# Performance work log

Hardware: AMD Instinct MI355X
Metric: run time of the kernel (lower is better)

## Reference

```python
import jax, jax.numpy as jnp
import numpy as np

B, N, D, H, E = 8, 2048, 128, 256, 524288
EPS = 1e-5

def setup_inputs() -> dict:
    key = jax.random.key(0)
    ks = jax.random.split(key, 16)
    def lin(k, fan_in, shape):
        b = 1.0 / np.sqrt(fan_in)
        return jax.random.uniform(k, shape, jnp.float32, -b, b)
    return {
        'x': jax.random.normal(ks[0], (B, N, 3), jnp.float32),
        'h': jax.random.normal(ks[1], (B, N, D), jnp.float32),
        'edge_indices': jax.random.randint(ks[2], (2, E), 0, B * N, jnp.int64),
        'batch_size': B,
        # filter_net: Linear(1,H) -> SiLU -> Linear(H,D)   (weights stored [in,out])
        'W1': lin(ks[3], 1, (1, H)), 'b1': lin(ks[4], 1, (H,)),
        'W2': lin(ks[5], H, (H, D)), 'b2': lin(ks[6], H, (D,)),
        # update_net: Linear(2D,H) -> LayerNorm(H) -> SiLU -> Linear(H,D)
        'W3': lin(ks[7], 2 * D, (2 * D, H)), 'b3': lin(ks[8], 2 * D, (H,)),
        'gamma': jnp.ones((H,), jnp.float32), 'beta': jnp.zeros((H,), jnp.float32),
        'W4': lin(ks[9], H, (H, D)), 'b4': lin(ks[10], H, (D,)),
    }

def reference(x, h, edge_indices, batch_size, W1, b1, W2, b2, W3, b3, gamma, beta, W4, b4):
    Bn, Nn, Dn = h.shape
    row, col = edge_indices[0], edge_indices[1]
    br, nr = row // Nn, row % Nn
    bc, nc = col // Nn, col % Nn
    x_row = x[br, nr]            # [E,3] gather
    x_col = x[bc, nc]            # [E,3]
    h_col = h[bc, nc]            # [E,D]
    diff = x_row - x_col
    dist = jnp.sqrt(jnp.sum(diff * diff, axis=-1, keepdims=True))  # [E,1]
    # distance-conditioned edge filter MLP
    edge_filters = jax.nn.silu(dist @ W1 + b1) @ W2 + b2           # [E,D]
    messages = h_col * edge_filters                                 # [E,D]
    # scatter-mean into B*N nodes (single-pass sum + count, clamp_min(1))
    n_tot = Bn * Nn
    sums = jax.ops.segment_sum(messages, row, num_segments=n_tot)
    counts = jax.ops.segment_sum(jnp.ones_like(row, dtype=messages.dtype), row, num_segments=n_tot)
    agg = (sums / jnp.maximum(counts, 1.0)[:, None]).reshape(Bn, Nn, Dn)
    # update MLP with LayerNorm
    u = jnp.concatenate([h, agg], axis=-1) @ W3 + b3               # [B,N,H]
    mu = jnp.mean(u, axis=-1, keepdims=True)
    var = jnp.mean((u - mu) ** 2, axis=-1, keepdims=True)
    un = (u - mu) * jax.lax.rsqrt(var + EPS) * gamma + beta
    return jax.nn.silu(un) @ W4 + b4                                # [B,N,D]
```

## Files before the change

kernel.cpp:

```cpp
#include <hip/hip_runtime.h>
#include <hip/hip_fp16.h>
#include <math.h>

#define BN_NODES 16384
#define DIM 128
#define HID 256
#define TK 4096
#define TRANGE 32.0f
#define TSTEP (TRANGE / (float)TK)
#define TINV  ((float)TK / TRANGE)
#define LN_EPS 1e-5f
#define EPB 4096
#define NBINS 1024
#define CAPB 768

typedef _Float16 f16x8 __attribute__((ext_vector_type(8)));
typedef __attribute__((ext_vector_type(4))) float f32x4;
typedef __attribute__((ext_vector_type(2))) float floatx2;
typedef __attribute__((ext_vector_type(8))) unsigned short ushort8v;

__device__ __forceinline__ unsigned short f2h(float f) {
    _Float16 h = (_Float16)f;
    return *(unsigned short*)&h;
}
__device__ __forceinline__ unsigned char f2fp8(float f) {
    unsigned int p = __builtin_amdgcn_cvt_pk_fp8_f32(f, f, 0, false);
    return (unsigned char)(p & 0xFFu);
}

__device__ __forceinline__ void acc8(uint2 q, uint2 tv, float* a) {
    floatx2 h01 = __builtin_amdgcn_cvt_pk_f32_fp8((int)q.x, false);
    floatx2 h23 = __builtin_amdgcn_cvt_pk_f32_fp8((int)q.x, true);
    floatx2 h45 = __builtin_amdgcn_cvt_pk_f32_fp8((int)q.y, false);
    floatx2 h67 = __builtin_amdgcn_cvt_pk_f32_fp8((int)q.y, true);
    floatx2 t01 = __builtin_amdgcn_cvt_pk_f32_fp8((int)tv.x, false);
    floatx2 t23 = __builtin_amdgcn_cvt_pk_f32_fp8((int)tv.x, true);
    floatx2 t45 = __builtin_amdgcn_cvt_pk_f32_fp8((int)tv.y, false);
    floatx2 t67 = __builtin_amdgcn_cvt_pk_f32_fp8((int)tv.y, true);
    a[0] = fmaf(h01[0], t01[0], a[0]);
    a[1] = fmaf(h01[1], t01[1], a[1]);
    a[2] = fmaf(h23[0], t23[0], a[2]);
    a[3] = fmaf(h23[1], t23[1], a[3]);
    a[4] = fmaf(h45[0], t45[0], a[4]);
    a[5] = fmaf(h45[1], t45[1], a[5]);
    a[6] = fmaf(h67[0], t67[0], a[6]);
    a[7] = fmaf(h67[1], t67[1], a[7]);
}

__device__ __forceinline__ void edge_one(const unsigned int* lrec, int idx, int dd,
        const unsigned char* __restrict__ xq,
        const unsigned char* __restrict__ Tb, float* a) {
    unsigned int r0 = lrec[idx];
    int c0 = (int)((r0 >> 12) & 0x3FFFu), k0 = (int)(r0 & 0xFFFu);
    uint2 q0 = *(const uint2*)&xq[c0 * DIM + dd];
    uint2 t0 = *(const uint2*)&Tb[k0 * DIM + dd];
    acc8(q0, t0, a);
}

__global__ __launch_bounds__(256) void prep_kernel(
        const float* __restrict__ W1, const float* __restrict__ b1,
        const float* __restrict__ W2, const float* __restrict__ b2,
        const float* __restrict__ W3, const float* __restrict__ W4,
        const float* __restrict__ h, const int* __restrict__ ei,
        const float* __restrict__ x,
        unsigned char* __restrict__ Tb, unsigned short* __restrict__ w3t,
        unsigned short* __restrict__ w4t, unsigned short* __restrict__ xh,
        unsigned char* __restrict__ xq, int* __restrict__ bin_cursor,
        unsigned int* __restrict__ staging, int nE) {
    __shared__ float smem[8 * 256 + 8 * 128];
    int bid = blockIdx.x, t = threadIdx.x;
    if (bid < 512) {
        float* a    = smem;
        float* part = smem + 8 * 256;
        int k0 = bid * 8;
        float w1 = W1[t], bb = b1[t];
#pragma unroll
        for (int k = 0; k < 8; ++k) {
            float dist = ((float)(k0 + k) + 0.5f) * TSTEP;
            float z = dist * w1 + bb;
            a[k * 256 + t] = z / (1.0f + expf(-z));
        }
        __syncthreads();
        int hg = t >> 7, d = t & 127;
        float acc[8] = {0.f,0.f,0.f,0.f,0.f,0.f,0.f,0.f};
        for (int hh = 0; hh < 128; ++hh) {
            int hidx = hg * 128 + hh;
            float w = W2[hidx * DIM + d];
#pragma unroll
            for (int k = 0; k < 8; ++k) acc[k] += a[k * 256 + hidx] * w;
        }
        if (hg == 1) {
#pragma unroll
            for (int k = 0; k < 8; ++k) part[k * 128 + d] = acc[k];
        }
        __syncthreads();
        if (hg == 0) {
            float bd = b2[d];
#pragma unroll
            for (int k = 0; k < 8; ++k)
                Tb[(k0 + k) * DIM + d] = f2fp8(acc[k] + part[k * 128 + d] + bd);
        }
    } else if (bid < 576) {
        float* s = smem;
        int tid = bid - 512, tr = tid >> 3, tc = tid & 7;
        int lr = t >> 5, lc = t & 31;
#pragma unroll
        for (int rep = 0; rep < 4; ++rep) {
            int k = tr * 32 + rep * 8 + lr, n = tc * 32 + lc;
            s[lc * 33 + rep * 8 + lr] = W3[k * 256 + n];
        }
        __syncthreads();
#pragma unroll
        for (int rep = 0; rep < 4; ++rep) {
            int n = tc * 32 + rep * 8 + lr, k = tr * 32 + lc;
            w3t[n * 256 + k] = f2h(s[(rep * 8 + lr) * 33 + lc]);
        }
    } else if (bid < 608) {
        float* s = smem;
        int tid = bid - 576, tr = tid >> 2, tc = tid & 3;
        int lr = t >> 5, lc = t & 31;
#pragma unroll
        for (int rep = 0; rep < 4; ++rep) {
            int k = tr * 32 + rep * 8 + lr, n = tc * 32 + lc;
            s[lc * 33 + rep * 8 + lr] = W4[k * 128 + n];
        }
        __syncthreads();
#pragma unroll
        for (int rep = 0; rep < 4; ++rep) {
            int n = tc * 32 + rep * 8 + lr, k = tr * 32 + lc;
            w4t[n * 256 + k] = f2h(s[(rep * 8 + lr) * 33 + lc]);
        }
    } else if (bid < 1632) {
        int i0 = (bid - 608) * 2048 + t * 8;
        float4 v0 = *(const float4*)&h[i0];
        float4 v1 = *(const float4*)&h[i0 + 4];
        ushort8v o;
        o[0] = f2h(v0.x); o[1] = f2h(v0.y); o[2] = f2h(v0.z); o[3] = f2h(v0.w);
        o[4] = f2h(v1.x); o[5] = f2h(v1.y); o[6] = f2h(v1.z); o[7] = f2h(v1.w);
        *(ushort8v*)&xh[i0] = o;
        unsigned int q0 = 0, q1 = 0;
        q0 = __builtin_amdgcn_cvt_pk_fp8_f32(v0.x, v0.y, q0, false);
        q0 = __builtin_amdgcn_cvt_pk_fp8_f32(v0.z, v0.w, q0, true);
        q1 = __builtin_amdgcn_cvt_pk_fp8_f32(v1.x, v1.y, q1, false);
        q1 = __builtin_amdgcn_cvt_pk_fp8_f32(v1.z, v1.w, q1, true);
        uint2 qq; qq.x = q0; qq.y = q1;
        *(uint2*)&xq[i0] = qq;
    } else {
        __shared__ int cnt[NBINS];
        __shared__ int pre[NBINS];
        __shared__ int gba[NBINS];
        __shared__ int sc[256];
        __shared__ unsigned int rec[EPB];
        int e0 = (bid - 1632) * EPB;
        int m = min(EPB, nE - e0);
        if (m < 0) m = 0;
#pragma unroll
        for (int j = 0; j < 4; ++j) cnt[j * 256 + t] = 0;
        __syncthreads();
        unsigned int code[16];
        int rk[16], bn[16];
#pragma unroll
        for (int j = 0; j < 16; ++j) {
            int idx = j * 256 + t;
            rk[j] = -1; bn[j] = 0; code[j] = 0;
            if (idx < m) {
                int e = e0 + idx;
                int r = ei[e], c = ei[nE + e];
                code[j] = ((unsigned int)r << 14) | (unsigned int)c;
                bn[j] = r >> 4;
                rk[j] = atomicAdd(&cnt[bn[j]], 1);
            }
        }
        __syncthreads();
        int c4[4], s4 = 0;
#pragma unroll
        for (int j = 0; j < 4; ++j) { c4[j] = cnt[t * 4 + j]; s4 += c4[j]; }
        sc[t] = s4;
        __syncthreads();
        for (int off = 1; off < 256; off <<= 1) {
            int v = (t >= off) ? sc[t - off] : 0;
            __syncthreads();
            sc[t] += v;
            __syncthreads();
        }
        int run = sc[t] - s4;
#pragma unroll
        for (int j = 0; j < 4; ++j) {
            int b = t * 4 + j;
            pre[b] = run; run += c4[j];
            gba[b] = atomicAdd(&bin_cursor[b], c4[j]);
        }
        __syncthreads();
#pragma unroll
        for (int j = 0; j < 16; ++j)
            if (rk[j] >= 0) rec[pre[bn[j]] + rk[j]] = code[j];
        __syncthreads();
        for (int i = t; i < m; i += 256) {
            unsigned int cd = rec[i];
            int b = (int)(cd >> 18);
            int r = (int)(cd >> 14);
            int c = (int)(cd & 0x3FFFu);
            float dx = x[r * 3 + 0] - x[c * 3 + 0];
            float dy = x[r * 3 + 1] - x[c * 3 + 1];
            float dz = x[r * 3 + 2] - x[c * 3 + 2];
            float u = sqrtf(dx * dx + dy * dy + dz * dz) * TINV;
            int k = min((int)u, TK - 1);
            unsigned int o = ((unsigned int)(r & 15) << 26)
                           | ((unsigned int)c << 12) | (unsigned int)k;
            int off = gba[b] + (i - pre[b]);
            if (off < CAPB) staging[b * CAPB + off] = o;
        }
    }
}

__global__ __launch_bounds__(512, 8) void mega_kernel(
        const unsigned int* __restrict__ staging, const int* __restrict__ bin_cursor,
        const unsigned char* __restrict__ Tb, const unsigned char* __restrict__ xq,
        const unsigned short* __restrict__ xh, const unsigned short* __restrict__ w3t,
        const float* __restrict__ b3, const float* __restrict__ gamma,
        const float* __restrict__ beta, const unsigned short* __restrict__ w4t,
        const float* __restrict__ b4, float* __restrict__ out) {
    __shared__ unsigned int lrec[CAPB];
    __shared__ int cnt16[16];
    __shared__ int pref[17];
    __shared__ int cur[16];
    __shared__ __align__(16) unsigned short aggh[16][136];
    __shared__ __align__(16) unsigned short a_lds[16][264];
    __shared__ float part_s[8][16], part_q[8][16];
    __shared__ float tot_mu[16], tot_rs[16];

    int t = threadIdx.x;
    int bin = blockIdx.x;
    int n0 = bin * 16;
    if (t < 16) cnt16[t] = 0;
    __syncthreads();
    int total = min(bin_cursor[bin], CAPB);
    long base = (long)bin * CAPB;

    unsigned int sr0 = 0, sr1 = 0;
    int have0 = (t < total), have1 = (t + 512 < total);
    if (have0) { sr0 = __builtin_nontemporal_load(&staging[base + t]);
                 atomicAdd(&cnt16[sr0 >> 26], 1); }
    if (have1) { sr1 = __builtin_nontemporal_load(&staging[base + t + 512]);
                 atomicAdd(&cnt16[sr1 >> 26], 1); }
    __syncthreads();
    if (t < 16) {
        int c = cnt16[t];
        int s = c;
#pragma unroll
        for (int off = 1; off < 16; off <<= 1) {
            int v = __shfl_up(s, off, 16);
            if (t >= off) s += v;
        }
        pref[t + 1] = s;
        cur[t] = s - c;
        if (t == 0) pref[0] = 0;
    }
    __syncthreads();

    if (have0) { int pos = atomicAdd(&cur[sr0 >> 26], 1); lrec[pos] = sr0; }
    if (have1) { int pos = atomicAdd(&cur[sr1 >> 26], 1); lrec[pos] = sr1; }
    __syncthreads();

    int wid = t >> 6, lane = t & 63;

    {
        int g = lane >> 4, l16 = lane & 15, dd = l16 * 8;
        int node = wid * 2 + (g >> 1);
        int sub = g & 1;
        int off = pref[node], len = pref[node + 1] - off;
        float a[8] = {0.f,0.f,0.f,0.f,0.f,0.f,0.f,0.f};
        int i = sub;
        for (; i + 2 < len; i += 4) {
            unsigned int r0 = lrec[off + i];
            unsigned int r1 = lrec[off + i + 2];
            int c0 = (int)((r0 >> 12) & 0x3FFFu), k0 = (int)(r0 & 0xFFFu);
            int c1 = (int)((r1 >> 12) & 0x3FFFu), k1 = (int)(r1 & 0xFFFu);
            uint2 q0 = *(const uint2*)&xq[c0 * DIM + dd];
            uint2 t0 = *(const uint2*)&Tb[k0 * DIM + dd];
            uint2 q1 = *(const uint2*)&xq[c1 * DIM + dd];
            uint2 t1 = *(const uint2*)&Tb[k1 * DIM + dd];
            acc8(q0, t0, a);
            acc8(q1, t1, a);
        }
        if (i < len)
            edge_one(lrec, off + i, dd, xq, Tb, a);
#pragma unroll
        for (int r = 0; r < 8; ++r) a[r] += __shfl_xor(a[r], 16, 64);
        if (sub == 0) {
            float inv = 1.0f / (float)max(len, 1);
            ushort8v o;
#pragma unroll
            for (int r = 0; r < 8; ++r) o[r] = f2h(a[r] * inv);
            *(ushort8v*)&aggh[node][dd] = o;
        }
    }
    __syncthreads();

    int wv = wid, q = lane >> 4, l15 = lane & 15;
    f32x4 acc[2];
    acc[0] = (f32x4){0.f, 0.f, 0.f, 0.f};
    acc[1] = (f32x4){0.f, 0.f, 0.f, 0.f};
    for (int kc = 0; kc < 8; ++kc) {
        f16x8 a;
        if (kc < 4) a = *(const f16x8*)&xh[(n0 + l15) * DIM + kc * 32 + q * 8];
        else        a = *(const f16x8*)&aggh[l15][(kc - 4) * 32 + q * 8];
#pragma unroll
        for (int nt = 0; nt < 2; ++nt) {
            f16x8 b = *(const f16x8*)&w3t[(wv * 32 + nt * 16 + l15) * 256 + kc * 32 + q * 8];
            acc[nt] = __builtin_amdgcn_mfma_f32_16x16x32_f16(a, b, acc[nt], 0, 0, 0);
        }
    }

    float b3v[2], gv[2], bvv[2];
#pragma unroll
    for (int nt = 0; nt < 2; ++nt) {
        int col = wv * 32 + nt * 16 + l15;
        b3v[nt] = b3[col]; gv[nt] = gamma[col]; bvv[nt] = beta[col];
    }
    {
        float s_[4], q_[4];
#pragma unroll
        for (int reg = 0; reg < 4; ++reg) {
            float su = 0.f, sq = 0.f;
#pragma unroll
            for (int nt = 0; nt < 2; ++nt) {
                float v = acc[nt][reg] + b3v[nt];
                acc[nt][reg] = v;
                su += v; sq += v * v;
            }
            s_[reg] = su; q_[reg] = sq;
        }
#pragma unroll
        for (int off = 1; off < 16; off <<= 1) {
#pragma unroll
            for (int reg = 0; reg < 4; ++reg) {
                s_[reg] += __shfl_xor(s_[reg], off, 64);
                q_[reg] += __shfl_xor(q_[reg], off, 64);
            }
        }
        if (l15 == 0) {
#pragma unroll
            for (int reg = 0; reg < 4; ++reg) {
                int r = q * 4 + reg;
                part_s[wv][r] = s_[reg];
                part_q[wv][r] = q_[reg];
            }
        }
    }
    __syncthreads();
    if (t < 16) {
        float st = 0.f, qt = 0.f;
#pragma unroll
        for (int w = 0; w < 8; ++w) { st += part_s[w][t]; qt += part_q[w][t]; }
        float mu = st * (1.0f / 256.0f);
        float var = qt * (1.0f / 256.0f) - mu * mu;
        tot_mu[t] = mu;
        tot_rs[t] = rsqrtf(var + LN_EPS);
    }
    __syncthreads();

#pragma unroll
    for (int reg = 0; reg < 4; ++reg) {
        int r = q * 4 + reg;
        float mu = tot_mu[r], rs = tot_rs[r];
#pragma unroll
        for (int nt = 0; nt < 2; ++nt) {
            float un = (acc[nt][reg] - mu) * rs * gv[nt] + bvv[nt];
            float act = un / (1.0f + expf(-un));
            a_lds[r][wv * 32 + nt * 16 + l15] = f2h(act);
        }
    }
    __syncthreads();

    f32x4 acc2 = (f32x4){0.f, 0.f, 0.f, 0.f};
    int col2 = wv * 16 + l15;
    for (int kc = 0; kc < 8; ++kc) {
        f16x8 a = *(const f16x8*)&a_lds[l15][kc * 32 + q * 8];
        f16x8 b = *(const f16x8*)&w4t[col2 * 256 + kc * 32 + q * 8];
        acc2 = __builtin_amdgcn_mfma_f32_16x16x32_f16(a, b, acc2, 0, 0, 0);
    }
    float b4v = b4[col2];
#pragma unroll
    for (int reg = 0; reg < 4; ++reg) {
        int node = n0 + q * 4 + reg;
        __builtin_nontemporal_store(acc2[reg] + b4v, &out[node * DIM + col2]);
    }
}

extern "C" void kernel_launch(void* const* d_in, const int* in_sizes, int n_in,
                              void* d_out, int out_size, void* d_ws, size_t ws_size,
                              hipStream_t stream) {
    const float* x     = (const float*)d_in[0];
    const float* h     = (const float*)d_in[1];
    const int*   ei    = (const int*)d_in[2];
    const float* W1    = (const float*)d_in[4];
    const float* b1    = (const float*)d_in[5];
    const float* W2    = (const float*)d_in[6];
    const float* b2    = (const float*)d_in[7];
    const float* W3    = (const float*)d_in[8];
    const float* b3    = (const float*)d_in[9];
    const float* gamma = (const float*)d_in[10];
    const float* beta  = (const float*)d_in[11];
    const float* W4    = (const float*)d_in[12];
    const float* b4    = (const float*)d_in[13];
    float* out = (float*)d_out;
    int nE = in_sizes[2] / 2;

    char* ws = (char*)d_ws;
    unsigned char*  Tb   = (unsigned char*)ws;  ws += (size_t)TK * DIM;
    unsigned short* w3t  = (unsigned short*)ws; ws += (size_t)HID * HID * 2;
    unsigned short* w4t  = (unsigned short*)ws; ws += (size_t)DIM * HID * 2;
    unsigned short* xh   = (unsigned short*)ws; ws += (size_t)BN_NODES * DIM * 2;
    unsigned char*  xq   = (unsigned char*)ws;  ws += (size_t)BN_NODES * DIM;
    int* bin_cursor = (int*)ws;                 ws += (size_t)NBINS * 4;
    unsigned int* staging = (unsigned int*)ws;  ws += (size_t)NBINS * CAPB * 4;

    int binBlocks = (nE + EPB - 1) / EPB;
    hipMemsetAsync(bin_cursor, 0, (size_t)NBINS * 4, stream);
    prep_kernel<<<1632 + binBlocks, 256, 0, stream>>>(W1, b1, W2, b2, W3, W4, h, ei, x,
                                                      Tb, w3t, w4t, xh, xq,
                                                      bin_cursor, staging, nE);
    mega_kernel<<<NBINS, 512, 0, stream>>>(staging, bin_cursor, Tb, xq, xh,
                                           w3t, b3, gamma, beta, w4t, b4, out);
}
```

Baseline: 155.8 us.

## Balance edge aggregation by splitting sorted edges evenly across groups with LDS atomics

Replaces per-node edge assignment (two 16-lane groups per node) with an even split of the bin's sorted edge list across 32 groups. Each group walks its contiguous range with a one-step software prefetch and flushes partial sums into a float LDS buffer via atomicAdd whenever the node changes. A separate pass then normalizes by count and converts to fp16. This targets load imbalance from uneven node degrees, at the cost of LDS atomics, an extra zero-init, an extra barrier and more shared memory.

```diff
diff --git a/kernel.cpp b/kernel.cpp
--- a/kernel.cpp
+++ b/kernel.cpp
@@ -18,6 +18,7 @@
 typedef __attribute__((ext_vector_type(4))) float f32x4;
 typedef __attribute__((ext_vector_type(2))) float floatx2;
 typedef __attribute__((ext_vector_type(8))) unsigned short ushort8v;
+typedef __attribute__((ext_vector_type(4))) unsigned short ushort4v;
 
 __device__ __forceinline__ unsigned short f2h(float f) {
     _Float16 h = (_Float16)f;
@@ -45,16 +46,6 @@
     a[5] = fmaf(h45[1], t45[1], a[5]);
     a[6] = fmaf(h67[0], t67[0], a[6]);
     a[7] = fmaf(h67[1], t67[1], a[7]);
-}
-
-__device__ __forceinline__ void edge_one(const unsigned int* lrec, int idx, int dd,
-        const unsigned char* __restrict__ xq,
-        const unsigned char* __restrict__ Tb, float* a) {
-    unsigned int r0 = lrec[idx];
-    int c0 = (int)((r0 >> 12) & 0x3FFFu), k0 = (int)(r0 & 0xFFFu);
-    uint2 q0 = *(const uint2*)&xq[c0 * DIM + dd];
-    uint2 t0 = *(const uint2*)&Tb[k0 * DIM + dd];
-    acc8(q0, t0, a);
 }
 
 __global__ __launch_bounds__(256) void prep_kernel(
@@ -223,7 +214,8 @@
     __shared__ unsigned int lrec[CAPB];
     __shared__ int cnt16[16];
     __shared__ int pref[17];
-    __shared__ int cur[16];
+    __shared__ int cur16[16];
+    __shared__ __align__(16) float aggf[16][128];
     __shared__ __align__(16) unsigned short aggh[16][136];
     __shared__ __align__(16) unsigned short a_lds[16][264];
     __shared__ float part_s[8][16], part_q[8][16];
@@ -233,6 +225,10 @@
     int bin = blockIdx.x;
     int n0 = bin * 16;
     if (t < 16) cnt16[t] = 0;
+    {
+        float4 z = (float4){0.f, 0.f, 0.f, 0.f};
+        *(float4*)&((float*)aggf)[t * 4] = z;
+    }
     __syncthreads();
     int total = min(bin_cursor[bin], CAPB);
     long base = (long)bin * CAPB;
@@ -253,49 +249,65 @@
             if (t >= off) s += v;
         }
         pref[t + 1] = s;
-        cur[t] = s - c;
+        cur16[t] = s - c;
         if (t == 0) pref[0] = 0;
     }
     __syncthreads();
 
-    if (have0) { int pos = atomicAdd(&cur[sr0 >> 26], 1); lrec[pos] = sr0; }
-    if (have1) { int pos = atomicAdd(&cur[sr1 >> 26], 1); lrec[pos] = sr1; }
+    if (have0) { int pos = atomicAdd(&cur16[sr0 >> 26], 1); lrec[pos] = sr0; }
+    if (have1) { int pos = atomicAdd(&cur16[sr1 >> 26], 1); lrec[pos] = sr1; }
+    __syncthreads();
+
+    {
+        int gg = t >> 4, l16 = t & 15, dd = l16 * 8;
+        int e0 = (gg * total) >> 5;
+        int e1 = ((gg + 1) * total) >> 5;
+        if (e0 < e1) {
+            float a[8] = {0.f,0.f,0.f,0.f,0.f,0.f,0.f,0.f};
+            unsigned int rec = lrec[e0];
+            int c = (int)((rec >> 12) & 0x3FFFu), k = (int)(rec & 0xFFFu);
+            uint2 q  = *(const uint2*)&xq[c * DIM + dd];
+            uint2 tv = *(const uint2*)&Tb[k * DIM + dd];
+            int cur = (int)(rec >> 26);
+            for (int i = e0; i < e1; ++i) {
+                unsigned int recn = 0;
+                uint2 qn, tn;
+                if (i + 1 < e1) {
+                    recn = lrec[i + 1];
+                    int cn = (int)((recn >> 12) & 0x3FFFu), kn = (int)(recn & 0xFFFu);
+                    qn = *(const uint2*)&xq[cn * DIM + dd];
+                    tn = *(const uint2*)&Tb[kn * DIM + dd];
+                }
+                int nd = (int)(rec >> 26);
+                if (nd != cur) {
+#pragma unroll
+                    for (int r = 0; r < 8; ++r) atomicAdd(&aggf[cur][dd + r], a[r]);
+#pragma unroll
+                    for (int r = 0; r < 8; ++r) a[r] = 0.f;
+                    cur = nd;
+                }
+                acc8(q, tv, a);
+                rec = recn; q = qn; tv = tn;
+            }
+#pragma unroll
+            for (int r = 0; r < 8; ++r) atomicAdd(&aggf[cur][dd + r], a[r]);
+        }
+    }
+    __syncthreads();
+
+    {
+        int idx = t * 4;
+        int node = idx >> 7, d0 = idx & 127;
+        float inv = 1.0f / (float)max(cnt16[node], 1);
+        float4 v = *(float4*)&((float*)aggf)[idx];
+        ushort4v o;
+        o[0] = f2h(v.x * inv); o[1] = f2h(v.y * inv);
+        o[2] = f2h(v.z * inv); o[3] = f2h(v.w * inv);
+        *(ushort4v*)&aggh[node][d0] = o;
+    }
     __syncthreads();
 
     int wid = t >> 6, lane = t & 63;
-
-    {
-        int g = lane >> 4, l16 = lane & 15, dd = l16 * 8;
-        int node = wid * 2 + (g >> 1);
-        int sub = g & 1;
-        int off = pref[node], len = pref[node + 1] - off;
-        float a[8] = {0.f,0.f,0.f,0.f,0.f,0.f,0.f,0.f};
-        int i = sub;
-        for (; i + 2 < len; i += 4) {
-            unsigned int r0 = lrec[off + i];
-            unsigned int r1 = lrec[off + i + 2];
-            int c0 = (int)((r0 >> 12) & 0x3FFFu), k0 = (int)(r0 & 0xFFFu);
-            int c1 = (int)((r1 >> 12) & 0x3FFFu), k1 = (int)(r1 & 0xFFFu);
-            uint2 q0 = *(const uint2*)&xq[c0 * DIM + dd];
-            uint2 t0 = *(const uint2*)&Tb[k0 * DIM + dd];
-            uint2 q1 = *(const uint2*)&xq[c1 * DIM + dd];
-            uint2 t1 = *(const uint2*)&Tb[k1 * DIM + dd];
-            acc8(q0, t0, a);
-            acc8(q1, t1, a);
-        }
-        if (i < len)
-            edge_one(lrec, off + i, dd, xq, Tb, a);
-#pragma unroll
-        for (int r = 0; r < 8; ++r) a[r] += __shfl_xor(a[r], 16, 64);
-        if (sub == 0) {
-            float inv = 1.0f / (float)max(len, 1);
-            ushort8v o;
-#pragma unroll
-            for (int r = 0; r < 8; ++r) o[r] = f2h(a[r] * inv);
-            *(ushort8v*)&aggh[node][dd] = o;
-        }
-    }
-    __syncthreads();
 
     int wv = wid, q = lane >> 4, l15 = lane & 15;
     f32x4 acc[2];
```

Result: slower. 174.6 us (+12.1%).
